# Kernel tuning notes

Measured on AMD Instinct MI355X. Metric: run time of the kernel, lower is better.

Reference implementation:

```python
import jax, jax.numpy as jnp
import numpy as np

SVL = 0.5        # spatial_volume_length
FVL = 0.86603    # frustum_volume_length
IMG = 256        # input_image_size
FD = 48          # frustum_volume_depth
FS = IMG // 8    # frustum_volume_size = 32


def grid_sample_3d(vol, grid):
    """Trilinear grid_sample, padding_mode='zeros', align_corners=True.
    vol: (B,C,Dv,Hv,Wv); grid: (B,D,H,W,3), last dim = (x,y,z) in [-1,1]
    where x indexes Wv, y indexes Hv, z indexes Dv. Returns (B,C,D,H,W)."""
    B, C, Dv, Hv, Wv = vol.shape
    sp = grid.shape[1:4]
    x = (grid[..., 0] + 1.0) * 0.5 * (Wv - 1)
    y = (grid[..., 1] + 1.0) * 0.5 * (Hv - 1)
    z = (grid[..., 2] + 1.0) * 0.5 * (Dv - 1)
    x0f, y0f, z0f = jnp.floor(x), jnp.floor(y), jnp.floor(z)
    xd, yd, zd = x - x0f, y - y0f, z - z0f
    x0, y0, z0 = x0f.astype(jnp.int32), y0f.astype(jnp.int32), z0f.astype(jnp.int32)
    vol_flat = vol.reshape(B, C, Dv * Hv * Wv)
    gather = jax.vmap(lambda vf, ix: vf[:, ix])  # (C,M),(K,) -> (C,K)
    out = jnp.zeros((B, C) + sp, vol.dtype)
    for dz in (0, 1):
        for dy in (0, 1):
            for dx in (0, 1):
                xi, yi, zi = x0 + dx, y0 + dy, z0 + dz
                valid = (xi >= 0) & (xi < Wv) & (yi >= 0) & (yi < Hv) & (zi >= 0) & (zi < Dv)
                w = ((xd if dx else 1.0 - xd)
                     * (yd if dy else 1.0 - yd)
                     * (zd if dz else 1.0 - zd))
                w = jnp.where(valid, w, 0.0)
                idx = ((jnp.clip(zi, 0, Dv - 1) * Hv + jnp.clip(yi, 0, Hv - 1)) * Wv
                       + jnp.clip(xi, 0, Wv - 1))
                g = gather(vol_flat, idx.reshape(B, -1)).reshape((B, C) + sp)
                out = out + w[:, None] * g
    return out


def setup_inputs() -> dict:
    key = jax.random.key(0)
    k1, k2, k3, k4 = jax.random.split(key, 4)
    B, N, TN, C, V = 2, 16, 8, 64, 32
    return {
        "spatial_volume": jax.random.normal(k1, (B, C, V, V, V), dtype=jnp.float32),
        "target_RT": jax.random.normal(k2, (B, N, 3, 4), dtype=jnp.float32),
        "target_K": jax.random.normal(k3, (B, N, 4, 4), dtype=jnp.float32),
        "target_indices": jax.random.randint(k4, (B, TN), 0, N),
    }


def reference(spatial_volume, target_RT, target_K, target_indices):
    B, C, V = spatial_volume.shape[0], spatial_volume.shape[1], spatial_volume.shape[2]
    TN = target_indices.shape[1]
    BT = B * TN
    H = W = FS
    D = FD
    dt = spatial_volume.dtype

    # camera centers: -R^T t, distances to origin
    R = target_RT[..., :3, :3]                  # B,N,3,3
    T = target_RT[..., :3, 3]                   # B,N,3
    cam_pos = -jnp.einsum('bnji,bnj->bni', R, T)
    cam_dist = jnp.linalg.norm(cam_pos, axis=-1)  # B,N

    # gather per-target-view pose / K / distance
    bidx = jnp.arange(B)[:, None]
    poses = target_RT[bidx, target_indices].reshape(BT, 3, 4)
    Ks = target_K[bidx, target_indices].reshape(BT, 4, 4)
    dist = cam_dist[bidx, target_indices].reshape(BT)
    near, far = dist - FVL, dist + FVL

    # per-ray depth values (constant across pixels since near/far are scalar per view)
    tlin = jnp.linspace(0.0, 1.0, D, dtype=dt)
    depth = near[:, None] + tlin[None, :] * (far - near)[:, None]   # BT,D

    # pixel grid at frustum resolution, scaled to input-image pixel coords
    ys, xs = jnp.meshgrid(jnp.arange(H, dtype=dt), jnp.arange(W, dtype=dt), indexing='ij')
    pix = jnp.stack([xs, ys, jnp.ones_like(xs)], 0).reshape(1, 3, H * W)
    scale = jnp.array([IMG / FS, IMG / FS, 1.0], dtype=dt).reshape(1, 3, 1)
    pix = pix * scale                                                # 1,3,HW
    pts = pix[:, :, None, :] * depth[:, None, :, None]               # BT,3,D,HW

    # unproject homogeneous image points through inverse(K @ [R|t])
    P = jnp.einsum('bij,bjk->bik', Ks[:, :3, :3], poses)             # BT,3,4
    bottom = jnp.broadcast_to(jnp.array([0.0, 0.0, 0.0, 1.0], dtype=dt).reshape(1, 1, 4), (BT, 1, 4))
    P4 = jnp.concatenate([P, bottom], axis=1)
    Pinv = jnp.linalg.inv(P4)
    xyz = jnp.einsum('bij,bjk->bik', Pinv[:, :3, :3], pts.reshape(BT, 3, D * H * W)) + Pinv[:, :3, 3:]

    # normalize world coords to [-1,1] of the spatial volume and sample
    grid = (xyz / SVL).reshape(BT, 3, D, H, W).transpose(0, 2, 3, 4, 1)  # BT,D,H,W,3
    sv = jnp.broadcast_to(spatial_volume[:, None], (B, TN, C, V, V, V)).reshape(BT, C, V, V, V)
    feats = grid_sample_3d(sv, grid)                                  # BT,C,D,H,W
    depth_vol = jnp.broadcast_to(depth[:, :, None, None], (BT, D, H, W))
    return feats, depth_vol
```

## Files before the change

kernel.cpp:

```cpp
#include <hip/hip_runtime.h>
#include <cstdint>

#define BB   2
#define NN   16
#define TNN  8
#define BT   16
#define CC   64
#define VV   32
#define V3   (VV*VV*VV)
#define DD   48
#define HH   32
#define WW   32
#define FVL_ 0.86603
#define DCH  4

__device__ void setup_one(int bt, const float* __restrict__ RT,
                          const float* __restrict__ Km,
                          const int* __restrict__ tidx, float* __restrict__ params) {
    int b = bt / TNN, j = bt % TNN;
    int n = tidx[b * TNN + j];
    const float* pose = RT + (size_t)(b * NN + n) * 12;
    const float* K    = Km + (size_t)(b * NN + n) * 16;

    double T0 = pose[3], T1 = pose[7], T2 = pose[11];
    double cp0 = -((double)pose[0] * T0 + (double)pose[4] * T1 + (double)pose[8]  * T2);
    double cp1 = -((double)pose[1] * T0 + (double)pose[5] * T1 + (double)pose[9]  * T2);
    double cp2 = -((double)pose[2] * T0 + (double)pose[6] * T1 + (double)pose[10] * T2);
    double dist = sqrt(cp0*cp0 + cp1*cp1 + cp2*cp2);
    double nearv = dist - FVL_;
    double step  = 2.0 * FVL_ / (DD - 1);

    double A[3][3], bv[3];
    #pragma unroll
    for (int i = 0; i < 3; ++i) {
        #pragma unroll
        for (int jj = 0; jj < 3; ++jj)
            A[i][jj] = (double)K[i*4+0]*pose[0*4+jj] + (double)K[i*4+1]*pose[1*4+jj]
                     + (double)K[i*4+2]*pose[2*4+jj];
        bv[i] = (double)K[i*4+0]*pose[3] + (double)K[i*4+1]*pose[7] + (double)K[i*4+2]*pose[11];
    }
    double c00 =  A[1][1]*A[2][2] - A[1][2]*A[2][1];
    double c01 =  A[1][2]*A[2][0] - A[1][0]*A[2][2];
    double c02 =  A[1][0]*A[2][1] - A[1][1]*A[2][0];
    double det = A[0][0]*c00 + A[0][1]*c01 + A[0][2]*c02;
    double Mi[3][3];
    Mi[0][0] = c00 / det;
    Mi[0][1] = (A[0][2]*A[2][1] - A[0][1]*A[2][2]) / det;
    Mi[0][2] = (A[0][1]*A[1][2] - A[0][2]*A[1][1]) / det;
    Mi[1][0] = c01 / det;
    Mi[1][1] = (A[0][0]*A[2][2] - A[0][2]*A[2][0]) / det;
    Mi[1][2] = (A[0][2]*A[1][0] - A[0][0]*A[1][2]) / det;
    Mi[2][0] = c02 / det;
    Mi[2][1] = (A[0][1]*A[2][0] - A[0][0]*A[2][1]) / det;
    Mi[2][2] = (A[0][0]*A[1][1] - A[0][1]*A[1][0]) / det;
    double tv[3];
    #pragma unroll
    for (int i = 0; i < 3; ++i)
        tv[i] = -(Mi[i][0]*bv[0] + Mi[i][1]*bv[1] + Mi[i][2]*bv[2]);

    const double s = 31.0;
    float* p = params + bt * 16;
    #pragma unroll
    for (int i = 0; i < 3; ++i) {
        p[i*4+0] = (float)(s * Mi[i][0] * 8.0);
        p[i*4+1] = (float)(s * Mi[i][1] * 8.0);
        p[i*4+2] = (float)(s * Mi[i][2]);
        p[i*4+3] = (float)(s * tv[i] + 15.5);
    }
    p[12] = (float)nearv;
    p[13] = (float)step;
}

__global__ void setup_params(const float* __restrict__ RT, const float* __restrict__ Km,
                             const int* __restrict__ tidx, float* __restrict__ params) {
    int bt = threadIdx.x;
    if (bt < BT) setup_one(bt, RT, Km, tidx, params);
}

__global__ __launch_bounds__(256) void prep_kernel(const float* __restrict__ vol,
                                                   ushort* __restrict__ volTb,
                                                   const float* __restrict__ RT,
                                                   const float* __restrict__ Km,
                                                   const int* __restrict__ tidx,
                                                   float* __restrict__ params) {
    if (blockIdx.x == BB * 512) {
        int bt = threadIdx.x;
        if (bt < BT) setup_one(bt, RT, Km, tidx, params);
        return;
    }
    __shared__ ushort tl[64 * 66];
    int b    = blockIdx.x >> 9;
    int tile = blockIdx.x & 511;
    size_t zyx0 = (size_t)tile << 6;
    int l  = threadIdx.x & 63;
    int gq = threadIdx.x >> 6;
    #pragma unroll
    for (int k = 0; k < 16; ++k) {
        int c = (gq << 4) + k;
        float v = vol[(((size_t)(b * 64 + c)) << 15) + zyx0 + l];
        uint32_t u = __float_as_uint(v);
        tl[l * 66 + c] = (ushort)((u + 0x7fffu + ((u >> 16) & 1u)) >> 16);
    }
    __syncthreads();
    #pragma unroll
    for (int k = 0; k < 16; ++k) {
        int zy = (gq << 4) + k;
        volTb[((size_t)b << 21) + ((zyx0 + zy) << 6) + l] = tl[zy * 66 + l];
    }
}

__global__ __launch_bounds__(512) void sample_bf16(const ushort* __restrict__ volTb,
                                                   const float* __restrict__ params,
                                                   float* __restrict__ feats,
                                                   float* __restrict__ depthv) {
    __shared__ float lds[64 * 65];
    int t   = threadIdx.x;
    int blk = blockIdx.x;
    int hp = blk & 15;
    int r  = blk >> 4;
    int dc = r & (DCH - 1);
    int bt = r / DCH;
    int b  = bt >> 3;

    const float* p = params + bt * 16;

    int lane = t & 63;
    int wv   = t >> 6;
    int pp   = lane >> 3;
    int q    = lane & 7;
    int pidx = (wv << 3) | pp;
    int w    = pidx & 31;
    int h0   = hp << 1;
    int h    = h0 | (pidx >> 5);

    float fw = (float)w, fh = (float)h;
    float Gx = fmaf(p[0], fw, fmaf(p[1], fh, p[2]));
    float Gy = fmaf(p[4], fw, fmaf(p[5], fh, p[6]));
    float Gz = fmaf(p[8], fw, fmaf(p[9], fh, p[10]));
    float px3 = p[3], py3 = p[7], pz3 = p[11];
    float nearv = p[12], step = p[13];

    const ushort* vb = volTb + ((size_t)b << 21) + (q << 3);

    int cA  = t >> 4;
    int p4A = t & 15;
    int cB  = cA + 32;
    size_t oBaseA = ((size_t)(bt * CC + cA) * DD) << 10;
    size_t oBaseB = ((size_t)(bt * CC + cB) * DD) << 10;
    size_t oTail  = (size_t)(h0 << 5);
    size_t dBase  = ((size_t)bt * DD) << 10;

    const int d0 = dc * (DD / DCH);
    for (int dd = 0; dd < DD / DCH; ++dd) {
        int d = d0 + dd;
        float depth = fmaf(step, (float)d, nearv);
        float cx = fmaf(depth, Gx, px3);
        float cy = fmaf(depth, Gy, py3);
        float cz = fmaf(depth, Gz, pz3);

        bool inside = (cx > -1.f) && (cx < 32.f) && (cy > -1.f) && (cy < 32.f)
                   && (cz > -1.f) && (cz < 32.f);

        float acc[8] = {0.f, 0.f, 0.f, 0.f, 0.f, 0.f, 0.f, 0.f};
        if (inside) {
            float xf = floorf(cx), yf = floorf(cy), zf = floorf(cz);
            int x0 = (int)xf, y0 = (int)yf, z0 = (int)zf;
            float xd = cx - xf, yd = cy - yf, zd = cz - zf;
            int x0c = max(x0, 0), x1c = min(x0 + 1, 31);
            int y0c = max(y0, 0), y1c = min(y0 + 1, 31);
            int z0c = max(z0, 0), z1c = min(z0 + 1, 31);
            float wx0 = (x0     >= 0)  ? 1.f - xd : 0.f;
            float wx1 = (x0 + 1 <= 31) ? xd       : 0.f;
            float wy0 = (y0     >= 0)  ? 1.f - yd : 0.f;
            float wy1 = (y0 + 1 <= 31) ? yd       : 0.f;
            float wz0 = (z0     >= 0)  ? 1.f - zd : 0.f;
            float wz1 = (z0 + 1 <= 31) ? zd       : 0.f;

            #define CORNER(zc, yc, xc, WGT) do {                                     \
                const uint4 v = *reinterpret_cast<const uint4*>(                      \
                    vb + ((((size_t)(zc) * 32 + (yc)) * 32 + (xc)) << 6));            \
                float wg = (WGT);                                                     \
                acc[0] = fmaf(wg, __uint_as_float(v.x << 16),          acc[0]);       \
                acc[1] = fmaf(wg, __uint_as_float(v.x & 0xffff0000u),  acc[1]);       \
                acc[2] = fmaf(wg, __uint_as_float(v.y << 16),          acc[2]);       \
                acc[3] = fmaf(wg, __uint_as_float(v.y & 0xffff0000u),  acc[3]);       \
                acc[4] = fmaf(wg, __uint_as_float(v.z << 16),          acc[4]);       \
                acc[5] = fmaf(wg, __uint_as_float(v.z & 0xffff0000u),  acc[5]);       \
                acc[6] = fmaf(wg, __uint_as_float(v.w << 16),          acc[6]);       \
                acc[7] = fmaf(wg, __uint_as_float(v.w & 0xffff0000u),  acc[7]);       \
            } while (0)
            CORNER(z0c, y0c, x0c, wz0 * wy0 * wx0);
            CORNER(z0c, y0c, x1c, wz0 * wy0 * wx1);
            CORNER(z0c, y1c, x0c, wz0 * wy1 * wx0);
            CORNER(z0c, y1c, x1c, wz0 * wy1 * wx1);
            CORNER(z1c, y0c, x0c, wz1 * wy0 * wx0);
            CORNER(z1c, y0c, x1c, wz1 * wy0 * wx1);
            CORNER(z1c, y1c, x0c, wz1 * wy1 * wx0);
            CORNER(z1c, y1c, x1c, wz1 * wy1 * wx1);
            #undef CORNER
        }

        int allout = __syncthreads_and((int)(!inside));
        size_t dOff = ((size_t)d) << 10;
        if (allout) {
            const float4 z4 = {0.f, 0.f, 0.f, 0.f};
            *reinterpret_cast<float4*>(&feats[oBaseA + dOff + oTail + (p4A << 2)]) = z4;
            *reinterpret_cast<float4*>(&feats[oBaseB + dOff + oTail + (p4A << 2)]) = z4;
        } else {
            #pragma unroll
            for (int j = 0; j < 8; ++j)
                lds[pidx * 65 + (q << 3) + j] = acc[j];
            __syncthreads();
            float4 v0, v1;
            v0.x = lds[(p4A * 4 + 0) * 65 + cA];
            v0.y = lds[(p4A * 4 + 1) * 65 + cA];
            v0.z = lds[(p4A * 4 + 2) * 65 + cA];
            v0.w = lds[(p4A * 4 + 3) * 65 + cA];
            v1.x = lds[(p4A * 4 + 0) * 65 + cB];
            v1.y = lds[(p4A * 4 + 1) * 65 + cB];
            v1.z = lds[(p4A * 4 + 2) * 65 + cB];
            v1.w = lds[(p4A * 4 + 3) * 65 + cB];
            *reinterpret_cast<float4*>(&feats[oBaseA + dOff + oTail + (p4A << 2)]) = v0;
            *reinterpret_cast<float4*>(&feats[oBaseB + dOff + oTail + (p4A << 2)]) = v1;
        }
        if (t < 16) {
            float depthb = fmaf(step, (float)d, nearv);
            float4 d4 = {depthb, depthb, depthb, depthb};
            reinterpret_cast<float4*>(&depthv[dBase + dOff + oTail])[t] = d4;
        }
    }
}

__global__ __launch_bounds__(512) void sample_fallback(const float* __restrict__ vol,
                                                       const float* __restrict__ params,
                                                       float* __restrict__ feats,
                                                       float* __restrict__ depthv) {
    int w  = threadIdx.x;
    int ty = threadIdx.y;
    int blk = blockIdx.x;
    int h  = blk & 31;
    int t2 = blk >> 5;
    int d  = t2 % DD;
    int bt = t2 / DD;
    int b  = bt >> 3;

    const float* p = params + bt * 16;
    float depth = fmaf(p[13], (float)d, p[12]);
    float fw = (float)w, fh = (float)h;
    float cx = fmaf(depth, fmaf(p[0], fw, fmaf(p[1], fh, p[2])),  p[3]);
    float cy = fmaf(depth, fmaf(p[4], fw, fmaf(p[5], fh, p[6])),  p[7]);
    float cz = fmaf(depth, fmaf(p[8], fw, fmaf(p[9], fh, p[10])), p[11]);

    float accs[4] = {0.f, 0.f, 0.f, 0.f};
    bool inside = (cx > -1.f) && (cx < 32.f) && (cy > -1.f) && (cy < 32.f)
               && (cz > -1.f) && (cz < 32.f);
    if (inside) {
        float xf = floorf(cx), yf = floorf(cy), zf = floorf(cz);
        int x0 = (int)xf, y0 = (int)yf, z0 = (int)zf;
        float xd = cx - xf, yd = cy - yf, zd = cz - zf;
        int x0c = max(x0, 0), x1c = min(x0 + 1, 31);
        int y0c = max(y0, 0), y1c = min(y0 + 1, 31);
        int z0c = max(z0, 0), z1c = min(z0 + 1, 31);
        float wx0 = (x0     >= 0)  ? 1.f - xd : 0.f;
        float wx1 = (x0 + 1 <= 31) ? xd       : 0.f;
        float wy0 = (y0     >= 0)  ? 1.f - yd : 0.f;
        float wy1 = (y0 + 1 <= 31) ? yd       : 0.f;
        float wz0 = (z0     >= 0)  ? 1.f - zd : 0.f;
        float wz1 = (z0 + 1 <= 31) ? zd       : 0.f;
        int o000 = ((z0c * 32) + y0c) * 32 + x0c;
        int o001 = ((z0c * 32) + y0c) * 32 + x1c;
        int o010 = ((z0c * 32) + y1c) * 32 + x0c;
        int o011 = ((z0c * 32) + y1c) * 32 + x1c;
        int o100 = ((z1c * 32) + y0c) * 32 + x0c;
        int o101 = ((z1c * 32) + y0c) * 32 + x1c;
        int o110 = ((z1c * 32) + y1c) * 32 + x0c;
        int o111 = ((z1c * 32) + y1c) * 32 + x1c;
        float w000 = wz0*wy0*wx0, w001 = wz0*wy0*wx1, w010 = wz0*wy1*wx0, w011 = wz0*wy1*wx1;
        float w100 = wz1*wy0*wx0, w101 = wz1*wy0*wx1, w110 = wz1*wy1*wx0, w111 = wz1*wy1*wx1;
        #pragma unroll
        for (int k = 0; k < 4; ++k) {
            const float* vc = vol + (size_t)(b * CC + (ty << 2) + k) * V3;
            float a = 0.f;
            a = fmaf(w000, vc[o000], a); a = fmaf(w001, vc[o001], a);
            a = fmaf(w010, vc[o010], a); a = fmaf(w011, vc[o011], a);
            a = fmaf(w100, vc[o100], a); a = fmaf(w101, vc[o101], a);
            a = fmaf(w110, vc[o110], a); a = fmaf(w111, vc[o111], a);
            accs[k] = a;
        }
    }
    const size_t CHs = (size_t)DD * HH * WW;
    size_t o = (((size_t)bt * CC + (ty << 2)) * DD + d) * (HH * WW) + h * WW + w;
    feats[o]           = accs[0];
    feats[o + CHs]     = accs[1];
    feats[o + 2 * CHs] = accs[2];
    feats[o + 3 * CHs] = accs[3];
    if (ty == 0)
        depthv[((size_t)bt * DD + d) * (HH * WW) + h * WW + w] = depth;
}

extern "C" void kernel_launch(void* const* d_in, const int* in_sizes, int n_in,
                              void* d_out, int out_size, void* d_ws, size_t ws_size,
                              hipStream_t stream) {
    const float* vol  = (const float*)d_in[0];
    const float* RT   = (const float*)d_in[1];
    const float* Km   = (const float*)d_in[2];
    const int*   tidx = (const int*)d_in[3];

    float* feats  = (float*)d_out;
    float* depthv = feats + (size_t)BT * CC * DD * HH * WW;

    float*  params = (float*)d_ws;
    ushort* volTb  = (ushort*)((char*)d_ws + 4096);
    const size_t volTb_bytes = (size_t)BB * CC * V3 * sizeof(ushort);
    bool use_cl = ws_size >= 4096 + volTb_bytes;

    if (use_cl) {
        prep_kernel<<<BB * 512 + 1, 256, 0, stream>>>(vol, volTb, RT, Km, tidx, params);
        sample_bf16<<<BT * 16 * DCH, 512, 0, stream>>>(volTb, params, feats, depthv);
    } else {
        setup_params<<<1, 64, 0, stream>>>(RT, Km, tidx, params);
        sample_fallback<<<BT * DD * HH, dim3(32, 16, 1), 0, stream>>>(vol, params, feats, depthv);
    }
}
```

Baseline: 212.7 us.

## Remap sample blocks to one depth slice each with whole-slice early-out

```diff
diff --git a/kernel.cpp b/kernel.cpp
--- a/kernel.cpp
+++ b/kernel.cpp
@@ -12,7 +12,6 @@
 #define HH   32
 #define WW   32
 #define FVL_ 0.86603
-#define DCH  4
 
 __device__ void setup_one(int bt, const float* __restrict__ RT,
                           const float* __restrict__ Km,
@@ -116,48 +115,73 @@
     __shared__ float lds[64 * 65];
     int t   = threadIdx.x;
     int blk = blockIdx.x;
-    int hp = blk & 15;
-    int r  = blk >> 4;
-    int dc = r & (DCH - 1);
-    int bt = r / DCH;
+    int d  = blk % DD;
+    int bt = blk / DD;
     int b  = bt >> 3;
 
     const float* p = params + bt * 16;
+    float depth = fmaf(p[13], (float)d, p[12]);
+    float p0 = p[0], p1 = p[1], p2 = p[2],  px3 = p[3];
+    float p4 = p[4], p5 = p[5], p6 = p[6],  py3 = p[7];
+    float p8 = p[8], p9 = p[9], p10 = p[10], pz3 = p[11];
+
+    bool in0, in1;
+    {
+        int i0 = t,        h0i = i0 >> 5, w0i = i0 & 31;
+        int i1 = t + 512,  h1i = i1 >> 5, w1i = i1 & 31;
+        float cx0 = fmaf(depth, fmaf(p0, (float)w0i, fmaf(p1, (float)h0i, p2)),  px3);
+        float cy0 = fmaf(depth, fmaf(p4, (float)w0i, fmaf(p5, (float)h0i, p6)),  py3);
+        float cz0 = fmaf(depth, fmaf(p8, (float)w0i, fmaf(p9, (float)h0i, p10)), pz3);
+        float cx1 = fmaf(depth, fmaf(p0, (float)w1i, fmaf(p1, (float)h1i, p2)),  px3);
+        float cy1 = fmaf(depth, fmaf(p4, (float)w1i, fmaf(p5, (float)h1i, p6)),  py3);
+        float cz1 = fmaf(depth, fmaf(p8, (float)w1i, fmaf(p9, (float)h1i, p10)), pz3);
+        in0 = (cx0 > -1.f) && (cx0 < 32.f) && (cy0 > -1.f) && (cy0 < 32.f)
+           && (cz0 > -1.f) && (cz0 < 32.f);
+        in1 = (cx1 > -1.f) && (cx1 < 32.f) && (cy1 > -1.f) && (cy1 < 32.f)
+           && (cz1 > -1.f) && (cz1 < 32.f);
+    }
+    int allout = __syncthreads_and((int)(!in0 && !in1));
+
+    const size_t base = (((size_t)(bt * CC)) * DD + d) << 10;
+
+    if (t < 256) {
+        float4 d4 = {depth, depth, depth, depth};
+        reinterpret_cast<float4*>(&depthv[(((size_t)bt * DD + d)) << 10])[t] = d4;
+    }
+
+    if (allout) {
+        const float4 z4 = {0.f, 0.f, 0.f, 0.f};
+        #pragma unroll
+        for (int i = 0; i < 32; ++i) {
+            int idx = (i << 9) | t;
+            int c   = idx >> 8;
+            int rem = idx & 255;
+            *reinterpret_cast<float4*>(&feats[base + (((size_t)c * DD) << 10) + (rem << 2)]) = z4;
+        }
+        return;
+    }
 
     int lane = t & 63;
     int wv   = t >> 6;
     int pp   = lane >> 3;
     int q    = lane & 7;
-    int pidx = (wv << 3) | pp;
-    int w    = pidx & 31;
-    int h0   = hp << 1;
-    int h    = h0 | (pidx >> 5);
-
-    float fw = (float)w, fh = (float)h;
-    float Gx = fmaf(p[0], fw, fmaf(p[1], fh, p[2]));
-    float Gy = fmaf(p[4], fw, fmaf(p[5], fh, p[6]));
-    float Gz = fmaf(p[8], fw, fmaf(p[9], fh, p[10]));
-    float px3 = p[3], py3 = p[7], pz3 = p[11];
-    float nearv = p[12], step = p[13];
-
+    int pin  = (wv << 3) | pp;
     const ushort* vb = volTb + ((size_t)b << 21) + (q << 3);
 
     int cA  = t >> 4;
     int p4A = t & 15;
     int cB  = cA + 32;
-    size_t oBaseA = ((size_t)(bt * CC + cA) * DD) << 10;
-    size_t oBaseB = ((size_t)(bt * CC + cB) * DD) << 10;
-    size_t oTail  = (size_t)(h0 << 5);
-    size_t dBase  = ((size_t)bt * DD) << 10;
-
-    const int d0 = dc * (DD / DCH);
-    for (int dd = 0; dd < DD / DCH; ++dd) {
-        int d = d0 + dd;
-        float depth = fmaf(step, (float)d, nearv);
-        float cx = fmaf(depth, Gx, px3);
-        float cy = fmaf(depth, Gy, py3);
-        float cz = fmaf(depth, Gz, pz3);
-
+    size_t oA = base + (((size_t)cA * DD) << 10);
+    size_t oB = base + (((size_t)cB * DD) << 10);
+
+    for (int ch = 0; ch < 16; ++ch) {
+        int pt = (ch << 6) | pin;
+        int w  = pt & 31;
+        int h  = pt >> 5;
+        float fw = (float)w, fh = (float)h;
+        float cx = fmaf(depth, fmaf(p0, fw, fmaf(p1, fh, p2)),  px3);
+        float cy = fmaf(depth, fmaf(p4, fw, fmaf(p5, fh, p6)),  py3);
+        float cz = fmaf(depth, fmaf(p8, fw, fmaf(p9, fh, p10)), pz3);
         bool inside = (cx > -1.f) && (cx < 32.f) && (cy > -1.f) && (cy < 32.f)
                    && (cz > -1.f) && (cz < 32.f);
 
@@ -200,34 +224,24 @@
             #undef CORNER
         }
 
-        int allout = __syncthreads_and((int)(!inside));
-        size_t dOff = ((size_t)d) << 10;
-        if (allout) {
-            const float4 z4 = {0.f, 0.f, 0.f, 0.f};
-            *reinterpret_cast<float4*>(&feats[oBaseA + dOff + oTail + (p4A << 2)]) = z4;
-            *reinterpret_cast<float4*>(&feats[oBaseB + dOff + oTail + (p4A << 2)]) = z4;
-        } else {
-            #pragma unroll
-            for (int j = 0; j < 8; ++j)
-                lds[pidx * 65 + (q << 3) + j] = acc[j];
-            __syncthreads();
-            float4 v0, v1;
-            v0.x = lds[(p4A * 4 + 0) * 65 + cA];
-            v0.y = lds[(p4A * 4 + 1) * 65 + cA];
-            v0.z = lds[(p4A * 4 + 2) * 65 + cA];
-            v0.w = lds[(p4A * 4 + 3) * 65 + cA];
-            v1.x = lds[(p4A * 4 + 0) * 65 + cB];
-            v1.y = lds[(p4A * 4 + 1) * 65 + cB];
-            v1.z = lds[(p4A * 4 + 2) * 65 + cB];
-            v1.w = lds[(p4A * 4 + 3) * 65 + cB];
-            *reinterpret_cast<float4*>(&feats[oBaseA + dOff + oTail + (p4A << 2)]) = v0;
-            *reinterpret_cast<float4*>(&feats[oBaseB + dOff + oTail + (p4A << 2)]) = v1;
-        }
-        if (t < 16) {
-            float depthb = fmaf(step, (float)d, nearv);
-            float4 d4 = {depthb, depthb, depthb, depthb};
-            reinterpret_cast<float4*>(&depthv[dBase + dOff + oTail])[t] = d4;
-        }
+        __syncthreads();
+        #pragma unroll
+        for (int j = 0; j < 8; ++j)
+            lds[pin * 65 + (q << 3) + j] = acc[j];
+        __syncthreads();
+
+        size_t cOff = (size_t)(ch << 6) + (size_t)(p4A << 2);
+        float4 v0, v1;
+        v0.x = lds[(p4A * 4 + 0) * 65 + cA];
+        v0.y = lds[(p4A * 4 + 1) * 65 + cA];
+        v0.z = lds[(p4A * 4 + 2) * 65 + cA];
+        v0.w = lds[(p4A * 4 + 3) * 65 + cA];
+        v1.x = lds[(p4A * 4 + 0) * 65 + cB];
+        v1.y = lds[(p4A * 4 + 1) * 65 + cB];
+        v1.z = lds[(p4A * 4 + 2) * 65 + cB];
+        v1.w = lds[(p4A * 4 + 3) * 65 + cB];
+        *reinterpret_cast<float4*>(&feats[oA + cOff]) = v0;
+        *reinterpret_cast<float4*>(&feats[oB + cOff]) = v1;
     }
 }
 
@@ -316,7 +330,7 @@
 
     if (use_cl) {
         prep_kernel<<<BB * 512 + 1, 256, 0, stream>>>(vol, volTb, RT, Km, tidx, params);
-        sample_bf16<<<BT * 16 * DCH, 512, 0, stream>>>(volTb, params, feats, depthv);
+        sample_bf16<<<BT * DD, 512, 0, stream>>>(volTb, params, feats, depthv);
     } else {
         setup_params<<<1, 64, 0, stream>>>(RT, Km, tidx, params);
         sample_fallback<<<BT * DD * HH, dim3(32, 16, 1), 0, stream>>>(vol, params, feats, depthv);
```

Result: no change. 213.2 us (+0.2%).
